# Kernel tuning notes

Hardware: AMD Instinct MI355X
Metric: run time of the kernel (lower is better)

Reference implementation:

```python
import jax, jax.numpy as jnp
import numpy as np

# ---- static configuration (mirrors init_kwargs) ----
B, V, C, NH, HD = 1, 6, 256, 8, 32     # batch, views, embed, heads, head_dim
Z, L, P = 4, 4, 2                       # z-ref points, fmap levels, ref points
BEV_H, BEV_W = 80, 80
Q = BEV_H * BEV_W
IMG_H, IMG_W = 480, 800
LEVEL_SHAPES = [(60, 100), (30, 50), (15, 25), (8, 13)]
S = sum(h * w for h, w in LEVEL_SHAPES)
RES = 0.512
OFFSET_SCALE = 1.0
FF = 512


def layer_norm(x, g, b):
    m = jnp.mean(x, -1, keepdims=True)
    v = jnp.var(x, -1, keepdims=True)
    return (x - m) / jnp.sqrt(v + 1e-5) * g + b


def _bev_grid():
    xs = (jnp.arange(BEV_W) + 0.5) / BEV_W
    ys = (jnp.arange(BEV_H) + 0.5) / BEV_H
    gy, gx = jnp.meshgrid(ys, xs, indexing='ij')
    ref = jnp.stack([gx.reshape(-1), gy.reshape(-1)], -1)        # (Q,2) normalized xy
    world = (ref - 0.5) * jnp.array([BEV_W * RES, BEV_H * RES])  # (Q,2) ego-frame meters
    return ref, world


def deform_sample(value, H, W, loc):
    """Bilinear sampling. value: (N, H*W, NH, HD); loc: (N, Qn, NH, PP, 2) in [0,1].
    Returns (N, Qn, NH, PP, HD); out-of-bounds samples contribute zero."""
    v = jnp.moveaxis(value, 2, 1)                                # (N, NH, HW, HD)
    x = loc[..., 0] * W - 0.5
    y = loc[..., 1] * H - 0.5
    x0 = jnp.floor(x); y0 = jnp.floor(y)
    lx, ly = x - x0, y - y0
    x0 = x0.astype(jnp.int32); y0 = y0.astype(jnp.int32)
    gather = jax.vmap(jax.vmap(lambda vt, it: vt[it]))           # over (N, NH)
    def corner(xi, yi, w):
        ok = ((xi >= 0) & (xi < W) & (yi >= 0) & (yi < H)).astype(value.dtype)
        idx = jnp.clip(yi, 0, H - 1) * W + jnp.clip(xi, 0, W - 1)
        g = gather(v, jnp.moveaxis(idx, 2, 1))                   # (N,NH,Qn,PP,HD)
        return jnp.moveaxis(g, 1, 2) * (w * ok)[..., None]
    return (corner(x0, y0, (1 - lx) * (1 - ly)) + corner(x0 + 1, y0, lx * (1 - ly))
            + corner(x0, y0 + 1, (1 - lx) * ly) + corner(x0 + 1, y0 + 1, lx * ly))


def _forward(bev_queries, bev_histories, multiscale_fmaps, transition_matrices, z_refs,
             cam_proj_matrices, Wv_t, Woff_t, boff_t, Ww_t, bw_t, Wo_t, bo_t, ln1_g, ln1_b,
             Wv_s, Woff_s, boff_s, Ww_s, bw_s, Wo_s, bo_s, ln2_g, ln2_b,
             W1, b1, W2, b2, ln3_g, ln3_b):
    ref, world = _bev_grid()
    q = bev_queries
    # ---------- temporal self-attention (deformable over current + warped history) ----------
    vcur = (q @ Wv_t).reshape(B, Q, NH, HD)
    vhist = (bev_histories @ Wv_t).reshape(B, Q, NH, HD)
    off_t = (q @ Woff_t + boff_t).reshape(B, Q, NH, 2, P, 2) * OFFSET_SCALE
    w_t = jax.nn.softmax((q @ Ww_t + bw_t).reshape(B, Q, NH, 2 * P), -1).reshape(B, Q, NH, 2, P)
    ext = jnp.array([BEV_W * RES, BEV_H * RES], jnp.float32)
    wh = jnp.concatenate([world, jnp.ones((Q, 1), jnp.float32)], -1)     # (Q,3)
    warped = jnp.einsum('bij,qj->bqi', transition_matrices, wh)          # (B,Q,3)
    ref_hist = warped[..., :2] / warped[..., 2:3] / ext + 0.5            # (B,Q,2)
    norm_bev = jnp.array([BEV_W, BEV_H], jnp.float32)
    loc_c = ref[None, :, None, None, :] + off_t[:, :, :, 0] / norm_bev
    loc_h = ref_hist[:, :, None, None, :] + off_t[:, :, :, 1] / norm_bev
    s_c = deform_sample(vcur, BEV_H, BEV_W, loc_c)                       # (B,Q,NH,P,HD)
    s_h = deform_sample(vhist, BEV_H, BEV_W, loc_h)
    out_t = (jnp.einsum('bqhp,bqhpd->bqhd', w_t[:, :, :, 0], s_c)
             + jnp.einsum('bqhp,bqhpd->bqhd', w_t[:, :, :, 1], s_h))
    out1 = out_t.reshape(B, Q, C) @ Wo_t + bo_t
    out2 = layer_norm(out1 + q, ln1_g, ln1_b)
    # ---------- spatial cross-attention (multi-view multi-scale deformable) ----------
    val = (multiscale_fmaps @ Wv_s).reshape(B * V, S, NH, HD)
    pts = jnp.concatenate([
        jnp.broadcast_to(world[:, None, :], (Q, Z, 2)),
        jnp.broadcast_to(z_refs[None, :, None], (Q, Z, 1)),
        jnp.ones((Q, Z, 1), jnp.float32)], -1)                           # (Q,Z,4) homogeneous
    uvd = jnp.einsum('vij,qzj->vqzi', cam_proj_matrices, pts)            # (V,Q,Z,3)
    d = uvd[..., 2]
    un = uvd[..., 0] / jnp.maximum(d, 1e-5) / IMG_W
    vn = uvd[..., 1] / jnp.maximum(d, 1e-5) / IMG_H
    valid = ((d > 1e-5) & (un >= 0) & (un <= 1) & (vn >= 0) & (vn <= 1)).astype(q.dtype)
    refuv = jnp.stack([un, vn], -1)                                      # (V,Q,Z,2)
    off_s = (out2 @ Woff_s + boff_s).reshape(B, Q, NH, Z, L, P, 2) * OFFSET_SCALE
    w_s = jax.nn.softmax((out2 @ Ww_s + bw_s).reshape(B, Q, NH, Z * L * P), -1)
    w_s = w_s.reshape(B, Q, NH, Z, L, P)
    acc = jnp.zeros((B, Q, NH, HD), q.dtype)
    start = 0
    for l, (Hl, Wl) in enumerate(LEVEL_SHAPES):
        vl = val[:, start:start + Hl * Wl]
        start += Hl * Wl
        loc = (refuv[None, :, :, None, :, None, :]
               + off_s[:, None, :, :, :, l] / jnp.array([Wl, Hl], jnp.float32))
        loc = jnp.broadcast_to(loc, (B, V, Q, NH, Z, P, 2)).reshape(B * V, Q, NH, Z * P, 2)
        samp = deform_sample(vl, Hl, Wl, loc).reshape(B, V, Q, NH, Z, P, HD)
        wl = w_s[:, None, :, :, :, l] * valid[None, :, :, None, :, None]
        acc = acc + jnp.einsum('bvqhzp,bvqhzpd->bqhd', wl, samp)
    count = jnp.maximum(valid.sum((0, 2)), 1.0)                          # (Q,) hit count
    out3 = (acc / count[None, :, None, None]).reshape(B, Q, C) @ Wo_s + bo_s
    out4 = layer_norm(out3 + out2, ln2_g, ln2_b)
    # ---------- feed-forward ----------
    out5 = jax.nn.relu(out4 @ W1 + b1) @ W2 + b2
    return layer_norm(out5 + out4, ln3_g, ln3_b)


def setup_inputs() -> dict:
    key = jax.random.key(0)
    ks = iter(jax.random.split(key, 40))
    def rn(shape, s=1.0):
        return jax.random.normal(next(ks), shape, jnp.float32) * s
    sc = 1.0 / float(np.sqrt(C))
    inp = {}
    inp['bev_queries'] = rn((B, Q, C), 0.1)
    inp['bev_histories'] = rn((B, Q, C), 0.1)
    inp['multiscale_fmaps'] = rn((B, V, S, C), 0.1)
    th = 0.02
    T = np.array([[np.cos(th), -np.sin(th), 0.5],
                  [np.sin(th), np.cos(th), 0.1],
                  [0.0, 0.0, 1.0]], np.float32)
    inp['transition_matrices'] = jnp.tile(jnp.asarray(T)[None], (B, 1, 1))
    inp['z_refs'] = jnp.linspace(-5.0, 3.0, Z).astype(jnp.float32)
    K = np.array([[400.0, 0.0, IMG_W / 2], [0.0, 400.0, IMG_H / 2], [0.0, 0.0, 1.0]], np.float32)
    Ps = []
    for vi in range(V):
        a = 2 * np.pi * vi / V
        Rt = np.zeros((3, 4), np.float32)
        Rt[0, :3] = [-np.sin(a), np.cos(a), 0.0]   # camera right
        Rt[1, :3] = [0.0, 0.0, -1.0]               # camera down
        Rt[2, :3] = [np.cos(a), np.sin(a), 0.0]    # camera forward
        Ps.append(K @ Rt)
    inp['cam_proj_matrices'] = jnp.asarray(np.stack(Ps))
    # temporal self-attention params
    inp['Wv_t'] = rn((C, C), sc)
    inp['Woff_t'] = rn((C, NH * 2 * P * 2), sc * 0.1)
    inp['boff_t'] = jnp.zeros((NH * 2 * P * 2,), jnp.float32)
    inp['Ww_t'] = rn((C, NH * 2 * P), sc)
    inp['bw_t'] = jnp.zeros((NH * 2 * P,), jnp.float32)
    inp['Wo_t'] = rn((C, C), sc)
    inp['bo_t'] = jnp.zeros((C,), jnp.float32)
    inp['ln1_g'] = jnp.ones((C,), jnp.float32)
    inp['ln1_b'] = jnp.zeros((C,), jnp.float32)
    # spatial cross-attention params
    inp['Wv_s'] = rn((C, C), sc)
    inp['Woff_s'] = rn((C, NH * Z * L * P * 2), sc * 0.1)
    inp['boff_s'] = jnp.zeros((NH * Z * L * P * 2,), jnp.float32)
    inp['Ww_s'] = rn((C, NH * Z * L * P), sc)
    inp['bw_s'] = jnp.zeros((NH * Z * L * P,), jnp.float32)
    inp['Wo_s'] = rn((C, C), sc)
    inp['bo_s'] = jnp.zeros((C,), jnp.float32)
    inp['ln2_g'] = jnp.ones((C,), jnp.float32)
    inp['ln2_b'] = jnp.zeros((C,), jnp.float32)
    # FFN params
    inp['W1'] = rn((C, FF), sc)
    inp['b1'] = jnp.zeros((FF,), jnp.float32)
    inp['W2'] = rn((FF, C), 1.0 / float(np.sqrt(FF)))
    inp['b2'] = jnp.zeros((C,), jnp.float32)
    inp['ln3_g'] = jnp.ones((C,), jnp.float32)
    inp['ln3_b'] = jnp.zeros((C,), jnp.float32)
    # static shape descriptors (treated as compile-time constants)
    inp['bev_spatial_shape'] = np.array([[BEV_H, BEV_W]], np.int64)
    inp['multiscale_fmap_shapes'] = np.array(LEVEL_SHAPES, np.int64)
    inp['img_spatial_shape'] = np.array([[IMG_H, IMG_W]], np.int64)
    return inp


def reference(bev_queries, bev_histories, multiscale_fmaps, transition_matrices, z_refs,
              cam_proj_matrices, Wv_t, Woff_t, boff_t, Ww_t, bw_t, Wo_t, bo_t, ln1_g, ln1_b,
              Wv_s, Woff_s, boff_s, Ww_s, bw_s, Wo_s, bo_s, ln2_g, ln2_b,
              W1, b1, W2, b2, ln3_g, ln3_b,
              bev_spatial_shape, multiscale_fmap_shapes, img_spatial_shape):
    return _forward(bev_queries, bev_histories, multiscale_fmaps, transition_matrices, z_refs,
                    cam_proj_matrices, Wv_t, Woff_t, boff_t, Ww_t, bw_t, Wo_t, bo_t, ln1_g, ln1_b,
                    Wv_s, Woff_s, boff_s, Ww_s, bw_s, Wo_s, bo_s, ln2_g, ln2_b,
                    W1, b1, W2, b2, ln3_g, ln3_b)
```

## Files before the change

### kernel.cpp

```cpp
#include <hip/hip_runtime.h>
#include <hip/hip_bf16.h>
#include <hip/hip_fp16.h>

typedef unsigned short u16;
typedef unsigned int u32;
typedef __attribute__((ext_vector_type(8))) _Float16 f16x8;
typedef __attribute__((ext_vector_type(4))) float f32x4;

#define Q_N  6400
#define S_N  7979
#define BEV  80

__device__ __forceinline__ float f16tof(u16 u) {
    __half h; *(u16*)&h = u; return __half2float(h);
}
__device__ __forceinline__ u16 ftof16(float f) {
    __half h = __float2half(f); return *(u16*)&h;
}

template <int AIN, int RELU, int OUTMODE, int SM4, int SM32>
__device__ __forceinline__ void gemm_body(
    const void* __restrict__ A, const u16* __restrict__ WT,
    const float* __restrict__ bias, const float* __restrict__ bias2,
    void* __restrict__ Cout, int M, int N, int K, int bx, int by,
    u16* Ah, u16* Wh)
{
    const int tid  = threadIdx.x;
    const int lane = tid & 63;
    const int wave = tid >> 6;
    const int wm = (wave >> 1) * 32, wn = (wave & 1) * 64;
    const int m0 = by * 64, n0 = bx * 128;
    const int arow = tid >> 2, ak = (tid & 3) * 8;
    const int wrow = tid >> 1, wk = (tid & 1) * 16;
    const int fr = lane & 15, g = lane >> 4;

    f32x4 acc[8];
    #pragma unroll
    for (int i = 0; i < 8; ++i) acc[i] = (f32x4)(0.f);

    for (int k0 = 0; k0 < K; k0 += 32) {
        {
            const bool okr = (m0 + arow) < M;
            u16* dh = &Ah[arow * 40 + ak];
            if (AIN == 0) {
                const float* ap = (const float*)A + (size_t)(m0 + arow) * K + k0 + ak;
                float4 v0 = okr ? *(const float4*)(ap)     : make_float4(0.f, 0.f, 0.f, 0.f);
                float4 v1 = okr ? *(const float4*)(ap + 4) : make_float4(0.f, 0.f, 0.f, 0.f);
                u16 hb[8];
                hb[0] = ftof16(v0.x); hb[1] = ftof16(v0.y);
                hb[2] = ftof16(v0.z); hb[3] = ftof16(v0.w);
                hb[4] = ftof16(v1.x); hb[5] = ftof16(v1.y);
                hb[6] = ftof16(v1.z); hb[7] = ftof16(v1.w);
                *(ushort4*)(dh)     = *(ushort4*)&hb[0];
                *(ushort4*)(dh + 4) = *(ushort4*)&hb[4];
            } else {
                const u16* ap = (const u16*)A + (size_t)(m0 + arow) * K + k0 + ak;
                uint4 u = okr ? *(const uint4*)ap : make_uint4(0, 0, 0, 0);
                *(uint4*)dh = u;
            }
        }
        {
            const size_t wo = (size_t)(n0 + wrow) * K + k0 + wk;
            *(uint4*)&Wh[wrow * 40 + wk]     = *(const uint4*)(WT + wo);
            *(uint4*)&Wh[wrow * 40 + wk + 8] = *(const uint4*)(WT + wo + 8);
        }
        __syncthreads();
        f16x8 fah[2], fwh[4];
        #pragma unroll
        for (int i = 0; i < 2; ++i)
            fah[i] = *(const f16x8*)&Ah[(wm + i * 16 + fr) * 40 + g * 8];
        #pragma unroll
        for (int j = 0; j < 4; ++j)
            fwh[j] = *(const f16x8*)&Wh[(wn + j * 16 + fr) * 40 + g * 8];
        #pragma unroll
        for (int i = 0; i < 2; ++i)
            #pragma unroll
            for (int j = 0; j < 4; ++j)
                acc[i * 4 + j] = __builtin_amdgcn_mfma_f32_16x16x32_f16(fah[i], fwh[j], acc[i * 4 + j], 0, 0, 0);
        __syncthreads();
    }
    const int g4r = g * 4;
    float bv[4];
    #pragma unroll
    for (int j = 0; j < 4; ++j) {
        int col = n0 + wn + j * 16 + fr;
        if (bias2) bv[j] = (col < 512) ? bias[col] : bias2[col - 512];
        else       bv[j] = bias ? bias[col] : 0.f;
    }
    const bool do_sm4  = SM4 && (wn == 64);
    #pragma unroll
    for (int i = 0; i < 2; ++i) {
        #pragma unroll
        for (int r = 0; r < 4; ++r) {
            const int row = m0 + wm + i * 16 + g4r + r;
            float v0 = acc[i * 4 + 0][r] + bv[0];
            float v1 = acc[i * 4 + 1][r] + bv[1];
            float v2 = acc[i * 4 + 2][r] + bv[2];
            float v3 = acc[i * 4 + 3][r] + bv[3];
            if (RELU) {
                v0 = fmaxf(v0, 0.f); v1 = fmaxf(v1, 0.f);
                v2 = fmaxf(v2, 0.f); v3 = fmaxf(v3, 0.f);
            }
            if (SM4 && do_sm4) {
                float m0q = fmaxf(v0, __shfl_xor(v0, 1));
                m0q = fmaxf(m0q, __shfl_xor(m0q, 2));
                float e0 = __expf(v0 - m0q);
                float s0 = e0 + __shfl_xor(e0, 1);
                s0 += __shfl_xor(s0, 2);
                v0 = e0 / s0;
                float m1q = fmaxf(v1, __shfl_xor(v1, 1));
                m1q = fmaxf(m1q, __shfl_xor(m1q, 2));
                float e1 = __expf(v1 - m1q);
                float s1 = e1 + __shfl_xor(e1, 1);
                s1 += __shfl_xor(s1, 2);
                v1 = e1 / s1;
                v2 = 0.f; v3 = 0.f;
            }
            if (row < M) {
                const int colb = n0 + wn + fr;
                if (OUTMODE == 1) {
                    u16* cp = (u16*)Cout + (size_t)row * N;
                    cp[colb]      = ftof16(v0);
                    cp[colb + 16] = ftof16(v1);
                    cp[colb + 32] = ftof16(v2);
                    cp[colb + 48] = ftof16(v3);
                } else {
                    float* cp = (float*)Cout + (size_t)row * N;
                    cp[colb]      = v0;
                    cp[colb + 16] = v1;
                    cp[colb + 32] = v2;
                    cp[colb + 48] = v3;
                }
            }
        }
    }
}

__global__ __launch_bounds__(256) void fused3_k(
    const float* __restrict__ fmaps, const float* __restrict__ q, const float* __restrict__ hist,
    const u16* __restrict__ Wv_s_h, const u16* __restrict__ Wv_t_h,
    const u16* __restrict__ Wc_h, const float* __restrict__ bc,
    u16* __restrict__ val_f16, u16* __restrict__ vcur, u16* __restrict__ vhist,
    float* __restrict__ owt)
{
    __shared__ u16 Ah[64 * 40], Wh[128 * 40];
    const int b = blockIdx.x;
    if (b < 1498) {
        gemm_body<0, 0, 1, 0, 0>(fmaps, Wv_s_h, nullptr, nullptr, val_f16,
                                 47874, 256, 256, b & 1, b >> 1, Ah, Wh);
    } else if (b < 1698) {
        int l = b - 1498;
        gemm_body<0, 0, 1, 0, 0>(q, Wv_t_h, nullptr, nullptr, vcur,
                                 6400, 256, 256, l & 1, l >> 1, Ah, Wh);
    } else if (b < 1898) {
        int l = b - 1698;
        gemm_body<0, 0, 1, 0, 0>(hist, Wv_t_h, nullptr, nullptr, vhist,
                                 6400, 256, 256, l & 1, l >> 1, Ah, Wh);
    } else {
        int l = b - 1898;
        gemm_body<0, 0, 0, 1, 0>(q, Wc_h, bc, nullptr, owt,
                                 6400, 128, 256, 0, l, Ah, Wh);
    }
}

template <int AIN, int RELU, int OUTMODE, int SM32, int STATS, int LNA>
__global__ __launch_bounds__(256, 4) void cgemm_k(
    const void* __restrict__ A, const u16* __restrict__ WT,
    const float* __restrict__ bias, const float* __restrict__ bias2,
    const float* __restrict__ res, float* __restrict__ rstat,
    const float* __restrict__ lng, const float* __restrict__ lnb,
    float* __restrict__ aux,
    void* __restrict__ Cout, int M, int N, int K)
{
    __shared__ u16 As[2][32 * 40];
    __shared__ u16 Wsh[2][64 * 40];
    const int tid  = threadIdx.x;
    const int lane = tid & 63;
    const int wave = tid >> 6;
    const int wm = (wave >> 1) * 16, wn = (wave & 1) * 32;
    const int fr = lane & 15, g = lane >> 4;
    const int nx = gridDim.x;
    const int nwg = nx * gridDim.y;
    const int o = blockIdx.y * nx + blockIdx.x;
    const int flat = (o & 7) * (nwg >> 3) + (o >> 3);
    const int bx = flat % nx, by = flat / nx;
    const int m0 = by * 32, n0 = bx * 64;
    const int ar = tid >> 3, ak = (tid & 7) * 4;
    const int wr = tid >> 2, wk = (tid & 3) * 8;
    const int NS = K >> 5;

    f32x4 acc[2] = {(f32x4)(0.f), (f32x4)(0.f)};

    const float* apf = (const float*)A + (size_t)(m0 + ar) * K + ak;
    const u16*  aph  = (const u16*)A + (size_t)(m0 + ar) * K + ak;
    const u16*  wp   = WT + (size_t)(n0 + wr) * K + wk;

    const float* rp = nullptr;
    float* auxp = nullptr;
    float mean = 0.f, rstd = 0.f;
    if (LNA) {
        rp = res + (size_t)(m0 + ar) * 256 + ak;
        if (bx == 0) auxp = aux + (size_t)(m0 + ar) * 256 + ak;
        const float sm = rstat[m0 + ar];
        const float sq = rstat[Q_N + m0 + ar];
        mean = sm * (1.f / 256.f);
        rstd = rsqrtf(sq * (1.f / 256.f) - mean * mean + 1e-5f);
    }

    if (AIN == 0) {
        float4 v = *(const float4*)apf;
        if (LNA) {
            float4 rr = *(const float4*)rp;
            float4 gg = *(const float4*)(lng + ak);
            float4 bb = *(const float4*)(lnb + ak);
            v.x = (v.x + rr.x - mean) * rstd * gg.x + bb.x;
            v.y = (v.y + rr.y - mean) * rstd * gg.y + bb.y;
            v.z = (v.z + rr.z - mean) * rstd * gg.z + bb.z;
            v.w = (v.w + rr.w - mean) * rstd * gg.w + bb.w;
            if (auxp) *(float4*)auxp = v;
        }
        u16 hb[4];
        hb[0] = ftof16(v.x); hb[1] = ftof16(v.y); hb[2] = ftof16(v.z); hb[3] = ftof16(v.w);
        *(ushort4*)&As[0][ar * 40 + ak] = *(ushort4*)&hb[0];
    } else {
        *(uint2*)&As[0][ar * 40 + ak] = *(const uint2*)aph;
    }
    *(uint4*)&Wsh[0][wr * 40 + wk] = *(const uint4*)wp;
    __syncthreads();

    for (int s = 0; s < NS; ++s) {
        float4 av; float4 rv; uint2 au; uint4 wv;
        const bool pf = (s + 1) < NS;
        if (pf) {
            if (AIN == 0) {
                av = *(const float4*)(apf + (s + 1) * 32);
                if (LNA) rv = *(const float4*)(rp + (s + 1) * 32);
            } else {
                au = *(const uint2*)(aph + (s + 1) * 32);
            }
            wv = *(const uint4*)(wp + (s + 1) * 32);
        }
        const int b = s & 1;
        f16x8 fa  = *(const f16x8*)&As[b][(wm + fr) * 40 + g * 8];
        f16x8 fw0 = *(const f16x8*)&Wsh[b][(wn + fr) * 40 + g * 8];
        f16x8 fw1 = *(const f16x8*)&Wsh[b][(wn + 16 + fr) * 40 + g * 8];
        acc[0] = __builtin_amdgcn_mfma_f32_16x16x32_f16(fa, fw0, acc[0], 0, 0, 0);
        acc[1] = __builtin_amdgcn_mfma_f32_16x16x32_f16(fa, fw1, acc[1], 0, 0, 0);
        if (pf) {
            const int nb = b ^ 1;
            if (AIN == 0) {
                if (LNA) {
                    const int ko = ak + (s + 1) * 32;
                    float4 gg = *(const float4*)(lng + ko);
                    float4 bb = *(const float4*)(lnb + ko);
                    av.x = (av.x + rv.x - mean) * rstd * gg.x + bb.x;
                    av.y = (av.y + rv.y - mean) * rstd * gg.y + bb.y;
                    av.z = (av.z + rv.z - mean) * rstd * gg.z + bb.z;
                    av.w = (av.w + rv.w - mean) * rstd * gg.w + bb.w;
                    if (auxp) *(float4*)(auxp + (s + 1) * 32) = av;
                }
                u16 hb[4];
                hb[0] = ftof16(av.x); hb[1] = ftof16(av.y);
                hb[2] = ftof16(av.z); hb[3] = ftof16(av.w);
                *(ushort4*)&As[nb][ar * 40 + ak] = *(ushort4*)&hb[0];
            } else {
                *(uint2*)&As[nb][ar * 40 + ak] = au;
            }
            *(uint4*)&Wsh[nb][wr * 40 + wk] = wv;
        }
        __syncthreads();
    }

    const int c0g = n0 + wn + fr, c1g = c0g + 16;
    float bv0, bv1;
    if (bias2) {
        bv0 = (c0g < 512) ? bias[c0g] : bias2[c0g - 512];
        bv1 = (c1g < 512) ? bias[c1g] : bias2[c1g - 512];
    } else {
        bv0 = bias ? bias[c0g] : 0.f;
        bv1 = bias ? bias[c1g] : 0.f;
    }
    const bool do_sm32 = SM32 && ((n0 + wn) >= 512);
    #pragma unroll
    for (int r = 0; r < 4; ++r) {
        const int row = m0 + wm + g * 4 + r;
        float v0 = acc[0][r] + bv0;
        float v1 = acc[1][r] + bv1;
        if (RELU) { v0 = fmaxf(v0, 0.f); v1 = fmaxf(v1, 0.f); }
        if (SM32 && do_sm32) {
            float ma = fmaxf(v0, v1);
            ma = fmaxf(ma, __shfl_xor(ma, 1));
            ma = fmaxf(ma, __shfl_xor(ma, 2));
            ma = fmaxf(ma, __shfl_xor(ma, 4));
            ma = fmaxf(ma, __shfl_xor(ma, 8));
            float e0 = __expf(v0 - ma), e1 = __expf(v1 - ma);
            float sa = e0 + e1;
            sa += __shfl_xor(sa, 1);
            sa += __shfl_xor(sa, 2);
            sa += __shfl_xor(sa, 4);
            sa += __shfl_xor(sa, 8);
            float ia = 1.f / sa;
            v0 = e0 * ia; v1 = e1 * ia;
        }
        if (STATS) {
            float t0 = v0 + res[(size_t)row * 256 + c0g];
            float t1 = v1 + res[(size_t)row * 256 + c1g];
            float s1v = t0 + t1;
            float s2v = t0 * t0 + t1 * t1;
            s1v += __shfl_xor(s1v, 1); s1v += __shfl_xor(s1v, 2);
            s1v += __shfl_xor(s1v, 4); s1v += __shfl_xor(s1v, 8);
            s2v += __shfl_xor(s2v, 1); s2v += __shfl_xor(s2v, 2);
            s2v += __shfl_xor(s2v, 4); s2v += __shfl_xor(s2v, 8);
            if (fr == 0) {
                atomicAdd(&rstat[row], s1v);
                atomicAdd(&rstat[Q_N + row], s2v);
            }
        }
        if (row < M) {
            if (OUTMODE == 1) {
                u16* cp = (u16*)Cout + (size_t)row * N;
                cp[c0g] = ftof16(v0);
                cp[c1g] = ftof16(v1);
            } else {
                float* cp = (float*)Cout + (size_t)row * N;
                cp[c0g] = v0;
                cp[c1g] = v1;
            }
        }
    }
}

__global__ __launch_bounds__(256) void wprep_k(
    const float* __restrict__ w0, const float* __restrict__ w1, const float* __restrict__ w2,
    const float* __restrict__ w3, const float* __restrict__ w4, const float* __restrict__ w5,
    const float* __restrict__ w6, const float* __restrict__ w7, u16* __restrict__ base,
    const float* __restrict__ Woff_t, const float* __restrict__ Ww_t,
    const float* __restrict__ boff_t, const float* __restrict__ bw_t,
    float* __restrict__ bc, float* __restrict__ st)
{
    const int b = blockIdx.x, tid = threadIdx.x;
    if (b >= 185) {
        st[(b - 185) * 256 + tid] = 0.f;
        return;
    }
    if (b == 184) {
        if (tid < 128) bc[tid] = (tid < 64) ? boff_t[tid] : (tid < 96 ? bw_t[tid - 64] : 0.f);
        return;
    }
    const int cum[10]  = {0, 16, 32, 48, 80, 96, 112, 144, 176, 184};
    const int Ks[9]    = {256, 256, 256, 256, 256, 256, 256, 512, 256};
    const int Ns[9]    = {256, 256, 256, 512, 256, 256, 512, 256, 128};
    const int hoff[9]  = {0, 65536, 131072, 196608, 327680, 393216, 458752, 589824, 720896};
    int seg = 0;
    #pragma unroll
    for (int s = 1; s < 9; ++s) if (b >= cum[s]) seg = s;
    const int K = Ks[seg], N = Ns[seg];
    const int t = b - cum[seg];
    const int ntn = N / 64;
    const int k0 = (t / ntn) * 64, n0 = (t % ntn) * 64;
    __shared__ float tile[64][65];
    const int rr = tid >> 2, cc = (tid & 3) * 16;
    if (seg < 8) {
        const float* W = seg == 0 ? w0 : seg == 1 ? w1 : seg == 2 ? w2 : seg == 3 ? w3 :
                         seg == 4 ? w4 : seg == 5 ? w5 : seg == 6 ? w6 : w7;
        #pragma unroll
        for (int c = 0; c < 4; ++c) {
            float4 v = *(const float4*)(W + (size_t)(k0 + rr) * N + n0 + cc + c * 4);
            tile[rr][cc + c * 4 + 0] = v.x;
            tile[rr][cc + c * 4 + 1] = v.y;
            tile[rr][cc + c * 4 + 2] = v.z;
            tile[rr][cc + c * 4 + 3] = v.w;
        }
    } else {
        #pragma unroll
        for (int i = 0; i < 16; ++i) {
            int n = n0 + cc + i, k = k0 + rr;
            float v = (n < 64) ? Woff_t[k * 64 + n] : (n < 96 ? Ww_t[k * 32 + n - 64] : 0.f);
            tile[rr][cc + i] = v;
        }
    }
    __syncthreads();
    const int nr = tid >> 2, kc = (tid & 3) * 16;
    u16 hb[16];
    #pragma unroll
    for (int i = 0; i < 16; ++i) hb[i] = ftof16(tile[kc + i][nr]);
    u16* hp = base + hoff[seg] + (size_t)(n0 + nr) * K + k0 + kc;
    *(ushort4*)(hp + 0)  = *(ushort4*)&hb[0];
    *(ushort4*)(hp + 4)  = *(ushort4*)&hb[4];
    *(ushort4*)(hp + 8)  = *(ushort4*)&hb[8];
    *(ushort4*)(hp + 12) = *(ushort4*)&hb[12];
}

__global__ __launch_bounds__(256) void ln_k(
    const float* __restrict__ x, const float* __restrict__ res,
    const float* __restrict__ g, const float* __restrict__ b,
    float* __restrict__ out)
{
    const int row = blockIdx.x, t = threadIdx.x;
    const size_t idx = (size_t)row * 256 + t;
    float v = x[idx] + res[idx];
    float s = v, ss = v * v;
    #pragma unroll
    for (int o = 32; o > 0; o >>= 1) {
        s += __shfl_down(s, o);
        ss += __shfl_down(ss, o);
    }
    __shared__ float red[8];
    __shared__ float mv[2];
    const int wv = t >> 6, ln = t & 63;
    if (ln == 0) { red[wv] = s; red[4 + wv] = ss; }
    __syncthreads();
    if (t == 0) {
        float S = red[0] + red[1] + red[2] + red[3];
        float SS = red[4] + red[5] + red[6] + red[7];
        float mean = S * (1.f / 256.f);
        float var = SS * (1.f / 256.f) - mean * mean;
        mv[0] = mean;
        mv[1] = rsqrtf(var + 1e-5f);
    }
    __syncthreads();
    out[idx] = (v - mv[0]) * mv[1] * g[t] + b[t];
}

__device__ __forceinline__ float4 bilin4h(const u16* __restrict__ v, int H, int W,
                                          float x, float y, int chb)
{
    float xf = floorf(x), yf = floorf(y);
    int x0 = (int)xf, y0 = (int)yf;
    int x1 = x0 + 1, y1 = y0 + 1;
    float fx = x - xf, fy = y - yf;
    float w00 = (1.f - fx) * (1.f - fy), w10 = fx * (1.f - fy);
    float w01 = (1.f - fx) * fy,         w11 = fx * fy;
    bool xi0 = (x0 >= 0) && (x0 < W);
    bool xi1 = (x1 >= 0) && (x1 < W);
    bool yi0 = (y0 >= 0) && (y0 < H);
    bool yi1 = (y1 >= 0) && (y1 < H);
    float4 r = make_float4(0.f, 0.f, 0.f, 0.f);
    #define CORNER(xi, yi, xx, yy, ww)                                           \
        if ((yi) && (xi)) {                                                      \
            uint2 u = *(const uint2*)(v + ((size_t)(yy) * W + (xx)) * 256 + chb);\
            float2 f0 = __half22float2(*(const __half2*)&u.x);                   \
            float2 f1 = __half22float2(*(const __half2*)&u.y);                   \
            r.x += (ww) * f0.x; r.y += (ww) * f0.y;                              \
            r.z += (ww) * f1.x; r.w += (ww) * f1.y;                              \
        }
    CORNER(xi0, yi0, x0, y0, w00)
    CORNER(xi1, yi0, x1, y0, w10)
    CORNER(xi0, yi1, x0, y1, w01)
    CORNER(xi1, yi1, x1, y1, w11)
    #undef CORNER
    return r;
}

__global__ __launch_bounds__(256) void temporal_k(
    const u16* __restrict__ vcur, const u16* __restrict__ vhist,
    const float* __restrict__ ow,
    const float* __restrict__ Tm, float* __restrict__ outt)
{
    const int b = blockIdx.x;
    const int q = (b & 7) * 800 + (b >> 3);
    const int tid = threadIdx.x;
    const int c4 = tid & 63, rep = tid >> 6;
    const int br = rep >> 1, p = rep & 1;
    const int h = c4 >> 3;
    const int chb = h * 32 + (c4 & 7) * 4;
    const int jx = q % BEV, iy = q / BEV;
    const float refx = (jx + 0.5f) / 80.f;
    const float refy = (iy + 0.5f) / 80.f;
    const float wx = (refx - 0.5f) * 40.96f;
    const float wy = (refy - 0.5f) * 40.96f;
    float bx, by;
    const u16* v;
    if (br == 0) { v = vcur; bx = refx; by = refy; }
    else {
        float h0 = Tm[0] * wx + Tm[1] * wy + Tm[2];
        float h1 = Tm[3] * wx + Tm[4] * wy + Tm[5];
        float h2 = Tm[6] * wx + Tm[7] * wy + Tm[8];
        v = vhist;
        bx = h0 / h2 / 40.96f + 0.5f;
        by = h1 / h2 / 40.96f + 0.5f;
    }
    const float* owq = ow + (size_t)q * 128;
    int ob = h * 8 + br * 4 + p * 2;
    float lx = bx + owq[ob] * (1.f / 80.f);
    float ly = by + owq[ob + 1] * (1.f / 80.f);
    float wgt = owq[64 + h * 4 + br * 2 + p];
    float4 sv = bilin4h(v, BEV, BEV, lx * 80.f - 0.5f, ly * 80.f - 0.5f, chb);
    __shared__ float4 s_acc[4][64];
    s_acc[rep][c4] = make_float4(wgt * sv.x, wgt * sv.y, wgt * sv.z, wgt * sv.w);
    __syncthreads();
    if (rep == 0) {
        float4 a = s_acc[0][c4], b2 = s_acc[1][c4], c = s_acc[2][c4], d = s_acc[3][c4];
        float4 o = make_float4(a.x + b2.x + c.x + d.x, a.y + b2.y + c.y + d.y,
                               a.z + b2.z + c.z + d.z, a.w + b2.w + c.w + d.w);
        *(float4*)(outt + (size_t)q * 256 + c4 * 4) = o;
    }
}

__global__ __launch_bounds__(256) void spatial_k(
    const u16* __restrict__ val, const u16* __restrict__ ow,
    const float* __restrict__ cam, const float* __restrict__ zrefs,
    float* __restrict__ out)
{
    const int b = blockIdx.x;
    const int q = (b & 7) * 800 + (b >> 3);
    const int tid = threadIdx.x;
    const int lane = tid & 63, wave = tid >> 6;
    const int hw = lane >> 5, lh = lane & 31;
    const int slot = wave * 2 + hw;
    const int h = lh >> 2, chb = h * 32 + (lh & 3) * 8;
    __shared__ float s_un[24], s_vn[24], s_ok[24];
    __shared__ int s_list[24];
    __shared__ int s_n;
    __shared__ float s_cnt;
    __shared__ float s_ox[256], s_oy[256], s_wt[256];
    __shared__ float s_part[8][256];
    const int jx = q % BEV, iy = q / BEV;
    const float wx = ((jx + 0.5f) / 80.f - 0.5f) * 40.96f;
    const float wy = ((iy + 0.5f) / 80.f - 0.5f) * 40.96f;
    if (tid < 24) {
        int v = tid >> 2, zz = tid & 3;
        float zr = zrefs[zz];
        const float* P = cam + v * 12;
        float u0 = P[0] * wx + P[1] * wy + P[2] * zr + P[3];
        float u1 = P[4] * wx + P[5] * wy + P[6] * zr + P[7];
        float dd = P[8] * wx + P[9] * wy + P[10] * zr + P[11];
        float dm = fmaxf(dd, 1e-5f);
        float un = u0 / dm / 800.f;
        float vn = u1 / dm / 480.f;
        bool ok = (dd > 1e-5f) && (un >= 0.f) && (un <= 1.f) && (vn >= 0.f) && (vn <= 1.f);
        s_un[tid] = un; s_vn[tid] = vn; s_ok[tid] = ok ? 1.f : 0.f;
    }
    {
        const u16* owq = ow + (size_t)q * 768;
        #pragma unroll
        for (int rep = 0; rep < 2; ++rep) {
            int flat = tid + rep * 256;
            int hh = flat >> 6, rem = flat & 63;
            int zz = rem >> 4, ll = (rem >> 2) & 3, pp = (rem >> 1) & 1, xy = rem & 1;
            int dst = (zz * 8 + ll * 2 + pp) * 8 + hh;
            float v = f16tof(owq[flat]);
            if (xy) s_oy[dst] = v; else s_ox[dst] = v;
        }
        int hh = tid >> 5, rem = tid & 31;
        s_wt[rem * 8 + hh] = f16tof(owq[512 + tid]);
    }
    __syncthreads();
    if (tid == 0) {
        int n = 0; float c = 0.f;
        for (int vz = 0; vz < 24; ++vz) {
            if (s_ok[vz] != 0.f) { s_list[n++] = vz; c += 1.f; }
        }
        s_n = n; s_cnt = fmaxf(c, 1.f);
    }
    __syncthreads();
    const int n4 = s_n * 4;
    float a0 = 0.f, a1 = 0.f, a2 = 0.f, a3 = 0.f, a4 = 0.f, a5 = 0.f, a6 = 0.f, a7 = 0.f;
    for (int w = slot; w < n4; w += 8) {
        const int it = w >> 2, l = w & 3;
        const int vz = s_list[it];
        const int v = vz >> 2, z = vz & 3;
        const float un = s_un[vz], vn = s_vn[vz];
        const int Hl  = (l == 0) ? 60  : (l == 1) ? 30   : (l == 2) ? 15   : 8;
        const int Wl  = (l == 0) ? 100 : (l == 1) ? 50   : (l == 2) ? 25   : 13;
        const int LSo = (l == 0) ? 0   : (l == 1) ? 6000 : (l == 2) ? 7500 : 7875;
        const u16* lv = val + ((size_t)v * S_N + LSo) * 256 + chb;
        const float unl = un * Wl - 0.5f, vnl = vn * Hl - 0.5f;
        const int Ws = Wl * 256;
        #pragma unroll
        for (int p = 0; p < 2; ++p) {
            const int idx = (z * 8 + l * 2 + p) * 8 + h;
            float x = unl + s_ox[idx];
            float y = vnl + s_oy[idx];
            float wgt = s_wt[idx];
            float xf = floorf(x), yf = floorf(y);
            int x0 = (int)xf, y0 = (int)yf;
            float fx = x - xf, fy = y - yf;
            bool xi0 = (x0 >= 0) & (x0 < Wl);
            bool xi1 = (x0 >= -1) & (x0 < Wl - 1);
            bool yi0 = (y0 >= 0) & (y0 < Hl);
            bool yi1 = (y0 >= -1) & (y0 < Hl - 1);
            int xc0 = min(max(x0, 0), Wl - 1);
            int xc1 = min(max(x0 + 1, 0), Wl - 1);
            int yc0 = min(max(y0, 0), Hl - 1);
            int yc1 = min(max(y0 + 1, 0), Hl - 1);
            float m00 = (xi0 & yi0) ? wgt : 0.f;
            float m10 = (xi1 & yi0) ? wgt : 0.f;
            float m01 = (xi0 & yi1) ? wgt : 0.f;
            float m11 = (xi1 & yi1) ? wgt : 0.f;
            __half2 w00 = __float2half2_rn((1.f - fx) * (1.f - fy) * m00);
            __half2 w10 = __float2half2_rn(fx * (1.f - fy) * m10);
            __half2 w01 = __float2half2_rn((1.f - fx) * fy * m01);
            __half2 w11 = __float2half2_rn(fx * fy * m11);
            const u16* r0p = lv + (size_t)yc0 * Ws;
            const u16* r1p = lv + (size_t)yc1 * Ws;
            uint4 u00 = *(const uint4*)(r0p + (size_t)xc0 * 256);
            uint4 u10 = *(const uint4*)(r0p + (size_t)xc1 * 256);
            uint4 u01 = *(const uint4*)(r1p + (size_t)xc0 * 256);
            uint4 u11 = *(const uint4*)(r1p + (size_t)xc1 * 256);
            __half2 h0 = __float2half2_rn(0.f), h1 = h0, h2 = h0, h3 = h0;
            {
                const __half2* hp = (const __half2*)&u00;
                h0 = __hfma2(w00, hp[0], h0); h1 = __hfma2(w00, hp[1], h1);
                h2 = __hfma2(w00, hp[2], h2); h3 = __hfma2(w00, hp[3], h3);
            }
            {
                const __half2* hp = (const __half2*)&u10;
                h0 = __hfma2(w10, hp[0], h0); h1 = __hfma2(w10, hp[1], h1);
                h2 = __hfma2(w10, hp[2], h2); h3 = __hfma2(w10, hp[3], h3);
            }
            {
                const __half2* hp = (const __half2*)&u01;
                h0 = __hfma2(w01, hp[0], h0); h1 = __hfma2(w01, hp[1], h1);
                h2 = __hfma2(w01, hp[2], h2); h3 = __hfma2(w01, hp[3], h3);
            }
            {
                const __half2* hp = (const __half2*)&u11;
                h0 = __hfma2(w11, hp[0], h0); h1 = __hfma2(w11, hp[1], h1);
                h2 = __hfma2(w11, hp[2], h2); h3 = __hfma2(w11, hp[3], h3);
            }
            float2 f0 = __half22float2(h0), f1 = __half22float2(h1);
            float2 f2 = __half22float2(h2), f3 = __half22float2(h3);
            a0 += f0.x; a1 += f0.y; a2 += f1.x; a3 += f1.y;
            a4 += f2.x; a5 += f2.y; a6 += f3.x; a7 += f3.y;
        }
    }
    *(float4*)&s_part[slot][chb]     = make_float4(a0, a1, a2, a3);
    *(float4*)&s_part[slot][chb + 4] = make_float4(a4, a5, a6, a7);
    __syncthreads();
    float sum = 0.f;
    #pragma unroll
    for (int k = 0; k < 8; ++k) sum += s_part[k][tid];
    out[(size_t)q * 256 + tid] = sum / s_cnt;
}

extern "C" void kernel_launch(void* const* d_in, const int* in_sizes, int n_in,
                              void* d_out, int out_size, void* d_ws, size_t ws_size,
                              hipStream_t stream) {
    (void)in_sizes; (void)n_in; (void)out_size; (void)ws_size;
    const float* q      = (const float*)d_in[0];
    const float* hist   = (const float*)d_in[1];
    const float* fmaps  = (const float*)d_in[2];
    const float* Tm     = (const float*)d_in[3];
    const float* zrefs  = (const float*)d_in[4];
    const float* cam    = (const float*)d_in[5];
    const float* Woff_t = (const float*)d_in[7];
    const float* boff_t = (const float*)d_in[8];
    const float* Ww_t   = (const float*)d_in[9];
    const float* bw_t   = (const float*)d_in[10];
    const float* bo_t   = (const float*)d_in[12];
    const float* ln1g   = (const float*)d_in[13];
    const float* ln1b   = (const float*)d_in[14];
    const float* boff_s = (const float*)d_in[17];
    const float* bw_s   = (const float*)d_in[19];
    const float* bo_s   = (const float*)d_in[21];
    const float* ln2g   = (const float*)d_in[22];
    const float* ln2b   = (const float*)d_in[23];
    const float* b1     = (const float*)d_in[25];
    const float* b2     = (const float*)d_in[27];
    const float* ln3g   = (const float*)d_in[28];
    const float* ln3b   = (const float*)d_in[29];

    float* ws    = (float*)d_ws;
    float* r0    = ws;
    float* r1    = ws + 1638400;
    float* owt   = ws + 3276800;
    float* r4    = ws + 4096000;
    u16*  r5u    = (u16*)(ws + 5734400);
    float* of4   = ws + 8192000;
    u16*  valbuf = (u16*)(ws + 9830400);
    u16*  vcur   = (u16*)(ws + 15958272);
    u16*  vhist  = (u16*)(ws + 16777472);
    u16*  wtab   = (u16*)(ws + 17596672);
    float* st1   = ws + 17973504;
    float* st2   = ws + 17986304;
    float* bc    = ws + 18350336;

    u16* hidden = valbuf;
    u16* Wv_t_h = wtab + 0;
    u16* Wo_t_h = wtab + 65536;
    u16* Wv_s_h = wtab + 131072;
    u16* Comb_h = wtab + 196608;
    u16* Wo_s_h = wtab + 393216;
    u16* W1_h   = wtab + 458752;
    u16* W2_h   = wtab + 589824;
    u16* Wc_h   = wtab + 720896;

    dim3 blk(256);
    auto gc = [](int M, int N) { return dim3((unsigned)(N / 64), (unsigned)((M + 31) / 32)); };

    wprep_k<<<dim3(285), blk, 0, stream>>>(
        (const float*)d_in[6], (const float*)d_in[11], (const float*)d_in[15],
        (const float*)d_in[16], (const float*)d_in[18], (const float*)d_in[20],
        (const float*)d_in[24], (const float*)d_in[26], wtab,
        Woff_t, Ww_t, boff_t, bw_t, bc, st1);
    fused3_k<<<dim3(1998), blk, 0, stream>>>(
        fmaps, q, hist, Wv_s_h, Wv_t_h, Wc_h, bc,
        valbuf, vcur, vhist, owt);
    temporal_k<<<dim3(6400), blk, 0, stream>>>(vcur, vhist, owt, Tm, r4);
    cgemm_k<0,0,0,0,1,0><<<gc(6400, 256), blk, 0, stream>>>(
        r4, Wo_t_h, bo_t, nullptr, q, st1, nullptr, nullptr, nullptr,
        r0, 6400, 256, 256);
    cgemm_k<0,0,1,1,0,1><<<gc(6400, 768), blk, 0, stream>>>(
        r0, Comb_h, boff_s, bw_s, q, st1, ln1g, ln1b, r1,
        r5u, 6400, 768, 256);
    spatial_k<<<dim3(6400), blk, 0, stream>>>(valbuf, r5u, cam, zrefs, r0);
    cgemm_k<0,0,0,0,1,0><<<gc(6400, 256), blk, 0, stream>>>(
        r0, Wo_s_h, bo_s, nullptr, r1, st2, nullptr, nullptr, nullptr,
        r4, 6400, 256, 256);
    cgemm_k<0,1,1,0,0,1><<<gc(6400, 512), blk, 0, stream>>>(
        r4, W1_h, b1, nullptr, r1, st2, ln2g, ln2b, of4,
        hidden, 6400, 512, 256);
    cgemm_k<1,0,0,0,0,0><<<gc(6400, 256), blk, 0, stream>>>(
        hidden, W2_h, b2, nullptr, nullptr, nullptr, nullptr, nullptr, nullptr,
        r0, 6400, 256, 512);
    ln_k<<<dim3(6400), blk, 0, stream>>>(r0, of4, ln3g, ln3b, (float*)d_out);
}
```

Measured before the change: 302.8 us.

## Precompute bilinear weights and offsets cooperatively in shared memory for spatial sampling

The spatial cross-attention sampler no longer has each 4-lane group redundantly recompute the bilinear corner weights, bounds masks and addresses. Each chunk of four view/z entries now first has all 256 threads compute one (point, head) sample's four half2 weights and four u32 offsets into shared memory. After a barrier, the lanes fetch those precomputed values and do only the gathers and FMAs. This removes redundant ALU work and uses 32-bit offsets, at the cost of two extra barriers per chunk and 8KB more shared memory.

Result: faster. 294.6 us (-2.7%).

```diff
diff --git a/kernel.cpp b/kernel.cpp
--- a/kernel.cpp
+++ b/kernel.cpp
@@ -515,6 +515,7 @@
     __shared__ float s_cnt;
     __shared__ float s_ox[256], s_oy[256], s_wt[256];
     __shared__ float s_part[8][256];
+    __shared__ __align__(16) u32 s_pre[256][8];
     const int jx = q % BEV, iy = q / BEV;
     const float wx = ((jx + 0.5f) / 80.f - 0.5f) * 40.96f;
     const float wy = ((iy + 0.5f) / 80.f - 0.5f) * 40.96f;
@@ -554,50 +555,62 @@
         s_n = n; s_cnt = fmaxf(c, 1.f);
     }
     __syncthreads();
-    const int n4 = s_n * 4;
+    const int nchunk = (s_n + 3) >> 2;
     float a0 = 0.f, a1 = 0.f, a2 = 0.f, a3 = 0.f, a4 = 0.f, a5 = 0.f, a6 = 0.f, a7 = 0.f;
-    for (int w = slot; w < n4; w += 8) {
-        const int it = w >> 2, l = w & 3;
-        const int vz = s_list[it];
-        const int v = vz >> 2, z = vz & 3;
-        const float un = s_un[vz], vn = s_vn[vz];
-        const int Hl  = (l == 0) ? 60  : (l == 1) ? 30   : (l == 2) ? 15   : 8;
-        const int Wl  = (l == 0) ? 100 : (l == 1) ? 50   : (l == 2) ? 25   : 13;
-        const int LSo = (l == 0) ? 0   : (l == 1) ? 6000 : (l == 2) ? 7500 : 7875;
-        const u16* lv = val + ((size_t)v * S_N + LSo) * 256 + chb;
-        const float unl = un * Wl - 0.5f, vnl = vn * Hl - 0.5f;
-        const int Ws = Wl * 256;
-        #pragma unroll
-        for (int p = 0; p < 2; ++p) {
-            const int idx = (z * 8 + l * 2 + p) * 8 + h;
-            float x = unl + s_ox[idx];
-            float y = vnl + s_oy[idx];
-            float wgt = s_wt[idx];
-            float xf = floorf(x), yf = floorf(y);
-            int x0 = (int)xf, y0 = (int)yf;
-            float fx = x - xf, fy = y - yf;
-            bool xi0 = (x0 >= 0) & (x0 < Wl);
-            bool xi1 = (x0 >= -1) & (x0 < Wl - 1);
-            bool yi0 = (y0 >= 0) & (y0 < Hl);
-            bool yi1 = (y0 >= -1) & (y0 < Hl - 1);
-            int xc0 = min(max(x0, 0), Wl - 1);
-            int xc1 = min(max(x0 + 1, 0), Wl - 1);
-            int yc0 = min(max(y0, 0), Hl - 1);
-            int yc1 = min(max(y0 + 1, 0), Hl - 1);
-            float m00 = (xi0 & yi0) ? wgt : 0.f;
-            float m10 = (xi1 & yi0) ? wgt : 0.f;
-            float m01 = (xi0 & yi1) ? wgt : 0.f;
-            float m11 = (xi1 & yi1) ? wgt : 0.f;
+    const u16* valc = val + chb;
+    for (int c = 0; c < nchunk; ++c) {
+        {
+            const int pi = tid >> 3, hh = tid & 7;
+            const int li = c * 4 + (pi >> 3);
+            const bool valid = li < s_n;
+            const int vz = s_list[valid ? li : 0];
+            const int v = vz >> 2, z = vz & 3;
+            const int l = (pi >> 1) & 3, p = pi & 1;
+            const int Hl  = (l == 0) ? 60  : (l == 1) ? 30   : (l == 2) ? 15   : 8;
+            const int Wl  = (l == 0) ? 100 : (l == 1) ? 50   : (l == 2) ? 25   : 13;
+            const int LSo = (l == 0) ? 0   : (l == 1) ? 6000 : (l == 2) ? 7500 : 7875;
+            const int idx = (z * 8 + l * 2 + p) * 8 + hh;
+            const float x = s_un[vz] * Wl - 0.5f + s_ox[idx];
+            const float y = s_vn[vz] * Hl - 0.5f + s_oy[idx];
+            const float wgt = valid ? s_wt[idx] : 0.f;
+            const float xf = floorf(x), yf = floorf(y);
+            const int x0 = (int)xf, y0 = (int)yf;
+            const float fx = x - xf, fy = y - yf;
+            const bool xi0 = (x0 >= 0) & (x0 < Wl);
+            const bool xi1 = (x0 >= -1) & (x0 < Wl - 1);
+            const bool yi0 = (y0 >= 0) & (y0 < Hl);
+            const bool yi1 = (y0 >= -1) & (y0 < Hl - 1);
+            const u32 xc0 = (u32)min(max(x0, 0), Wl - 1) << 8;
+            const u32 xc1 = (u32)min(max(x0 + 1, 0), Wl - 1) << 8;
+            const u32 base = (u32)(v * S_N + LSo) << 8;
+            const u32 r0o = base + ((u32)(min(max(y0, 0), Hl - 1) * Wl) << 8);
+            const u32 r1o = base + ((u32)(min(max(y0 + 1, 0), Hl - 1) * Wl) << 8);
+            const float m00 = (xi0 & yi0) ? wgt : 0.f;
+            const float m10 = (xi1 & yi0) ? wgt : 0.f;
+            const float m01 = (xi0 & yi1) ? wgt : 0.f;
+            const float m11 = (xi1 & yi1) ? wgt : 0.f;
             __half2 w00 = __float2half2_rn((1.f - fx) * (1.f - fy) * m00);
             __half2 w10 = __float2half2_rn(fx * (1.f - fy) * m10);
             __half2 w01 = __float2half2_rn((1.f - fx) * fy * m01);
             __half2 w11 = __float2half2_rn(fx * fy * m11);
-            const u16* r0p = lv + (size_t)yc0 * Ws;
-            const u16* r1p = lv + (size_t)yc1 * Ws;
-            uint4 u00 = *(const uint4*)(r0p + (size_t)xc0 * 256);
-            uint4 u10 = *(const uint4*)(r0p + (size_t)xc1 * 256);
-            uint4 u01 = *(const uint4*)(r1p + (size_t)xc0 * 256);
-            uint4 u11 = *(const uint4*)(r1p + (size_t)xc1 * 256);
+            u32* pre = s_pre[tid];
+            pre[0] = *(u32*)&w00; pre[1] = *(u32*)&w10;
+            pre[2] = *(u32*)&w01; pre[3] = *(u32*)&w11;
+            pre[4] = r0o + xc0;   pre[5] = r0o + xc1;
+            pre[6] = r1o + xc0;   pre[7] = r1o + xc1;
+        }
+        __syncthreads();
+        #pragma unroll
+        for (int j = 0; j < 4; ++j) {
+            const u32* pre = s_pre[(slot * 4 + j) * 8 + h];
+            uint4 wv = *(const uint4*)(pre);
+            uint4 ov = *(const uint4*)(pre + 4);
+            uint4 u00 = *(const uint4*)(valc + ov.x);
+            uint4 u10 = *(const uint4*)(valc + ov.y);
+            uint4 u01 = *(const uint4*)(valc + ov.z);
+            uint4 u11 = *(const uint4*)(valc + ov.w);
+            __half2 w00 = *(__half2*)&wv.x, w10 = *(__half2*)&wv.y;
+            __half2 w01 = *(__half2*)&wv.z, w11 = *(__half2*)&wv.w;
             __half2 h0 = __float2half2_rn(0.f), h1 = h0, h2 = h0, h3 = h0;
             {
                 const __half2* hp = (const __half2*)&u00;
@@ -624,6 +637,7 @@
             a0 += f0.x; a1 += f0.y; a2 += f1.x; a3 += f1.y;
             a4 += f2.x; a5 += f2.y; a6 += f3.x; a7 += f3.y;
         }
+        __syncthreads();
     }
     *(float4*)&s_part[slot][chb]     = make_float4(a0, a1, a2, a3);
     *(float4*)&s_part[slot][chb + 4] = make_float4(a4, a5, a6, a7);
```
